# Optimization experiments

Hardware: AMD Instinct MI355X
Metric: run time of the kernel (lower is better)

Reference implementation:

```python
import jax, jax.numpy as jnp
import numpy as np

N, D, V = 16384, 2048, 8192  # rows, code bits, val_range (codebook size)


def setup_inputs() -> dict:
    key = jax.random.key(0)
    k1, k2 = jax.random.split(key)
    x = jax.random.normal(k1, (N, D), dtype=jnp.float32)   # encoded rows
    di = jax.random.normal(k2, (D, V), dtype=jnp.float32)  # decode codebook (fwd.di)
    return {"x": x, "di": di}


def reference(x, di):
    # Original loops over rows doing (1,D)@(D,V) then argmax; batched this is one
    # GEMM [N,D]@[D,V] -> [N,V] followed by argmax over the V axis, cast to float32
    # (the torch code stores the index into a float32 output tensor).
    scores = jnp.matmul(x, di)                  # [N, V]
    return jnp.argmax(scores, axis=1).astype(jnp.float32)  # [N]
```

## Files before the change

### kernel.cpp

```cpp
#include <hip/hip_runtime.h>

typedef _Float16 f16x8 __attribute__((ext_vector_type(8)));
typedef float f32x4 __attribute__((ext_vector_type(4)));
typedef float f32x16 __attribute__((ext_vector_type(16)));
typedef int i32x4 __attribute__((ext_vector_type(4)));
typedef int i32x8 __attribute__((ext_vector_type(8)));

__device__ __forceinline__ unsigned int fkey(float f) {
    unsigned int u = __float_as_uint(f);
    return u ^ ((u & 0x80000000u) ? 0xFFFFFFFFu : 0x80000000u);
}
__device__ __forceinline__ float unkey(unsigned int k) {
    unsigned int u = (k & 0x80000000u) ? (k ^ 0x80000000u) : ~k;
    return __uint_as_float(u);
}

__device__ __forceinline__ unsigned int f32_to_e4m3(float f) {
    float a = fabsf(f);
    a = fminf(a, 448.0f);
    unsigned int s = (__float_as_uint(f) >> 24) & 0x80u;
    if (a < 0.015625f) {
        int m = (int)rintf(a * 512.0f);
        return s | (unsigned int)m;
    }
    int e = ilogbf(a);
    float step = ldexpf(1.0f, e - 3);
    int q = (int)rintf(a / step);
    if (q == 16) { e += 1; q = 8; }
    return s | (unsigned int)(((e + 7) << 3) | (q - 8));
}

__global__ __launch_bounds__(256) void prep_x_q(
    const float* __restrict__ x, unsigned char* __restrict__ Xq)
{
    size_t base = ((size_t)blockIdx.x * 256 + threadIdx.x) * 8;
    float4 a0 = *(const float4*)(x + base);
    float4 a1 = *(const float4*)(x + base + 4);
    float v[8] = {a0.x, a0.y, a0.z, a0.w, a1.x, a1.y, a1.z, a1.w};
    unsigned long long b = 0;
#pragma unroll
    for (int j = 0; j < 8; ++j)
        b |= (unsigned long long)f32_to_e4m3(v[j]) << (8 * j);
    *(unsigned long long*)(Xq + base) = b;
}

__global__ __launch_bounds__(256) void prep_di_q(
    const float* __restrict__ di, unsigned char* __restrict__ DqT,
    _Float16* __restrict__ DhT, _Float16* __restrict__ DlT, int D, int V)
{
    int v  = blockIdx.x * 64 + (threadIdx.x & 63);
    int d0 = blockIdx.y * 32 + (threadIdx.x >> 6) * 8;
    f16x8 h, l;
    unsigned long long b = 0;
#pragma unroll
    for (int j = 0; j < 8; ++j) {
        float val = di[(size_t)(d0 + j) * V + v];
        _Float16 hh = (_Float16)val;
        h[j] = hh;
        l[j] = (_Float16)(val - (float)hh);
        b |= (unsigned long long)f32_to_e4m3(val) << (8 * j);
    }
    *(unsigned long long*)(DqT + (size_t)v * D + d0) = b;
    *(f16x8*)(DhT + (size_t)v * D + d0) = h;
    *(f16x8*)(DlT + (size_t)v * D + d0) = l;
}

__global__ __launch_bounds__(512, 1) void gemm_mx_top2(
    const unsigned char* __restrict__ Xq, const unsigned char* __restrict__ DqT,
    unsigned long long* __restrict__ cand, int N, int D, int V)
{
    __shared__ __align__(16) unsigned char sm[65536];

    const int tid = threadIdx.x;
    const int w = tid >> 6, lane = tid & 63;
    const int wr = w >> 2, wc = w & 3;
    const int l31 = lane & 31, hl = lane >> 5;

    const int cpx = gridDim.x >> 3;
    const int swz = (blockIdx.x & 7) * cpx + (blockIdx.x >> 3);
    const int bm = (swz >> 5) * 256;
    const int bn = (swz & 31) * 256;

    const int srow_in = lane >> 2;
    const int sp      = lane & 3;
    auto stage = [&](int buf, int k0) {
#pragma unroll
        for (int i = 0; i < 4; ++i) {
            const int g = w * 4 + i;
            const int op = g >> 4;
            const int c  = g & 15;
            const int row = c * 16 + srow_in;
            const int slog = sp ^ ((row >> 1) & 3);
            const unsigned char* src =
                (op ? DqT + (size_t)(bn + row) * D : Xq + (size_t)(bm + row) * D)
                + k0 + slog * 16;
            __builtin_amdgcn_global_load_lds(
                (const __attribute__((address_space(1))) void*)src,
                (__attribute__((address_space(3))) void*)
                    (sm + buf * 32768 + op * 16384 + c * 1024),
                16, 0, 0);
        }
    };
    auto ldfrag = [&](int buf, int op, int r) -> i32x8 {
        const unsigned char* base =
            sm + buf * 32768 + op * 16384 + (r >> 4) * 1024 + (r & 15) * 64;
        const int sw = (r >> 1) & 3;
        i32x4 lo = *(const i32x4*)(base + (((hl << 1)    ) ^ sw) * 16);
        i32x4 hi = *(const i32x4*)(base + (((hl << 1) | 1) ^ sw) * 16);
        return __builtin_shufflevector(lo, hi, 0, 1, 2, 3, 4, 5, 6, 7);
    };

    f32x16 acc[4][2];
#pragma unroll
    for (int fm = 0; fm < 4; ++fm)
#pragma unroll
        for (int fn = 0; fn < 2; ++fn)
#pragma unroll
            for (int q = 0; q < 16; ++q) acc[fm][fn][q] = 0.0f;

    const int nt = D / 64;
    int cb = 0;

    stage(0, 0);
    __syncthreads();

#pragma unroll 1
    for (int t = 0; t < nt; ++t) {
        if (t + 1 < nt) stage(cb ^ 1, (t + 1) * 64);

        i32x8 b0 = ldfrag(cb, 1, wc * 64 + 0 * 32 + l31);
        i32x8 b1 = ldfrag(cb, 1, wc * 64 + 1 * 32 + l31);
#pragma unroll
        for (int fm = 0; fm < 4; ++fm) {
            i32x8 a = ldfrag(cb, 0, wr * 128 + fm * 32 + l31);
            acc[fm][0] = __builtin_amdgcn_mfma_scale_f32_32x32x64_f8f6f4(
                a, b0, acc[fm][0], 0, 0, 0, 0x7F7F7F7F, 0, 0x7F7F7F7F);
            acc[fm][1] = __builtin_amdgcn_mfma_scale_f32_32x32x64_f8f6f4(
                a, b1, acc[fm][1], 0, 0, 0, 0x7F7F7F7F, 0, 0x7F7F7F7F);
        }
        __syncthreads();
        cb ^= 1;
    }

    const int nblk = V >> 8;
    const int blkn = bn >> 8;
#pragma unroll
    for (int fm = 0; fm < 4; ++fm)
#pragma unroll
        for (int j = 0; j < 16; ++j) {
            const int row = bm + wr * 128 + fm * 32 + (j & 3) + 8 * (j >> 2) + 4 * hl;
            const int c0 = bn + wc * 64 + l31;
            unsigned long long p0 =
                ((unsigned long long)fkey(acc[fm][0][j]) << 32) |
                (unsigned long long)(0xFFFFFFFFu - (unsigned int)c0);
            unsigned long long p1 =
                ((unsigned long long)fkey(acc[fm][1][j]) << 32) |
                (unsigned long long)(0xFFFFFFFFu - (unsigned int)(c0 + 32));
            unsigned long long t1 = p0 > p1 ? p0 : p1;
            unsigned long long t2 = p0 > p1 ? p1 : p0;
#pragma unroll
            for (int m = 1; m < 32; m <<= 1) {
                unsigned long long o1 = __shfl_xor(t1, m);
                unsigned long long o2 = __shfl_xor(t2, m);
                unsigned long long n1 = t1 > o1 ? t1 : o1;
                unsigned long long lo = t1 > o1 ? o1 : t1;
                unsigned long long m2 = t2 > o2 ? t2 : o2;
                t2 = lo > m2 ? lo : m2;
                t1 = n1;
            }
            if (l31 == 0) {
                size_t ci = (((size_t)row * nblk + blkn) * 4 + wc) * 2;
                cand[ci] = t1;
                cand[ci + 1] = t2;
            }
        }
}

#define DELTA 16.5f

__global__ __launch_bounds__(256) void refine_kernel(
    const unsigned long long* __restrict__ cand,
    const float* __restrict__ X,
    const _Float16* __restrict__ DhT, const _Float16* __restrict__ DlT,
    float* __restrict__ out, int N, int D, int V)
{
    const int w = threadIdx.x >> 6, lane = threadIdx.x & 63;
    const int r = blockIdx.x * 4 + w;
    if (r >= N) return;

    const int nent = (V >> 8) * 8;
    const unsigned long long* cr = cand + (size_t)r * nent;

    unsigned long long p[4];
#pragma unroll
    for (int i = 0; i < 4; ++i) p[i] = cr[lane * 4 + i];

    unsigned long long pmax = p[0];
#pragma unroll
    for (int i = 1; i < 4; ++i) if (p[i] > pmax) pmax = p[i];
#pragma unroll
    for (int m = 1; m < 64; m <<= 1) {
        unsigned long long o = __shfl_xor(pmax, m);
        if (o > pmax) pmax = o;
    }

    const float s1 = unkey((unsigned int)(pmax >> 32));
    const unsigned int kthr = fkey(s1 - DELTA);

    int cnt = 0;
    unsigned long long masks[4];
#pragma unroll
    for (int i = 0; i < 4; ++i) {
        masks[i] = __ballot((unsigned int)(p[i] >> 32) >= kthr);
        cnt += __popcll(masks[i]);
    }

    if (cnt <= 1) {
        if (lane == 0)
            out[r] = (float)(0xFFFFFFFFu - (unsigned int)(pmax & 0xFFFFFFFFull));
        return;
    }

    const float* xrow = X + (size_t)r * D;
    float xbuf[32];
#pragma unroll
    for (int q = 0; q < 8; ++q) {
        float4 xv = *(const float4*)(xrow + lane * 32 + q * 4);
        xbuf[q * 4 + 0] = xv.x; xbuf[q * 4 + 1] = xv.y;
        xbuf[q * 4 + 2] = xv.z; xbuf[q * 4 + 3] = xv.w;
    }

    unsigned long long bestp = 0;
    for (int i = 0; i < 4; ++i) {
        unsigned long long mask = masks[i];
        while (mask) {
            const int src = __ffsll((unsigned long long)mask) - 1;
            mask &= mask - 1;
            const unsigned long long cp = __shfl(p[i], src);
            const int col = (int)(0xFFFFFFFFu - (unsigned int)(cp & 0xFFFFFFFFull));

            const f16x8* dh = (const f16x8*)(DhT + (size_t)col * D) + lane * 4;
            const f16x8* dl = (const f16x8*)(DlT + (size_t)col * D) + lane * 4;
            float s = 0.0f;
#pragma unroll
            for (int q = 0; q < 4; ++q) {
                f16x8 h = dh[q], l = dl[q];
#pragma unroll
                for (int e = 0; e < 8; ++e)
                    s = fmaf(xbuf[q * 8 + e], (float)h[e] + (float)l[e], s);
            }
#pragma unroll
            for (int m = 1; m < 64; m <<= 1) s += __shfl_xor(s, m);

            const unsigned long long pp =
                ((unsigned long long)fkey(s) << 32) |
                (unsigned long long)(0xFFFFFFFFu - (unsigned int)col);
            if (pp > bestp) bestp = pp;
        }
    }
    if (lane == 0)
        out[r] = (float)(0xFFFFFFFFu - (unsigned int)(bestp & 0xFFFFFFFFull));
}

#define FBK 16
#define FTM 8
#define FTN 8

__global__ __launch_bounds__(256) void gemm_argmax_fp32_kernel(
    const float* __restrict__ A, const float* __restrict__ B,
    unsigned long long* __restrict__ best, int N, int D, int V)
{
    __shared__ float As[FBK][128 + 4];
    __shared__ float Bs[FBK][128 + 4];

    const int tid = threadIdx.x;
    const int tx = tid & 15;
    const int ty = tid >> 4;
    const int bm = blockIdx.y * 128;
    const int bn = blockIdx.x * 128;

    const int arow  = tid >> 2;
    const int acol4 = tid & 3;
    const int brow  = tid >> 5;
    const int bcol4 = tid & 31;

    float acc[FTM][FTN];
#pragma unroll
    for (int i = 0; i < FTM; ++i)
#pragma unroll
        for (int j = 0; j < FTN; ++j) acc[i][j] = 0.0f;

    for (int k0 = 0; k0 < D; k0 += FBK) {
        float4 a0 = *reinterpret_cast<const float4*>(&A[(size_t)(bm + arow) * D + k0 + acol4 * 4]);
        float4 a1 = *reinterpret_cast<const float4*>(&A[(size_t)(bm + arow + 64) * D + k0 + acol4 * 4]);
        float4 b0 = *reinterpret_cast<const float4*>(&B[(size_t)(k0 + brow) * V + bn + bcol4 * 4]);
        float4 b1 = *reinterpret_cast<const float4*>(&B[(size_t)(k0 + brow + 8) * V + bn + bcol4 * 4]);

        As[acol4 * 4 + 0][arow] = a0.x;
        As[acol4 * 4 + 1][arow] = a0.y;
        As[acol4 * 4 + 2][arow] = a0.z;
        As[acol4 * 4 + 3][arow] = a0.w;
        As[acol4 * 4 + 0][arow + 64] = a1.x;
        As[acol4 * 4 + 1][arow + 64] = a1.y;
        As[acol4 * 4 + 2][arow + 64] = a1.z;
        As[acol4 * 4 + 3][arow + 64] = a1.w;
        *reinterpret_cast<float4*>(&Bs[brow][bcol4 * 4]) = b0;
        *reinterpret_cast<float4*>(&Bs[brow + 8][bcol4 * 4]) = b1;

        __syncthreads();
#pragma unroll
        for (int kk = 0; kk < FBK; ++kk) {
            float4 av0 = *reinterpret_cast<const float4*>(&As[kk][ty * FTM]);
            float4 av1 = *reinterpret_cast<const float4*>(&As[kk][ty * FTM + 4]);
            float4 bv0 = *reinterpret_cast<const float4*>(&Bs[kk][tx * FTN]);
            float4 bv1 = *reinterpret_cast<const float4*>(&Bs[kk][tx * FTN + 4]);
            float a[FTM] = {av0.x, av0.y, av0.z, av0.w, av1.x, av1.y, av1.z, av1.w};
            float b[FTN] = {bv0.x, bv0.y, bv0.z, bv0.w, bv1.x, bv1.y, bv1.z, bv1.w};
#pragma unroll
            for (int i = 0; i < FTM; ++i)
#pragma unroll
                for (int j = 0; j < FTN; ++j)
                    acc[i][j] = fmaf(a[i], b[j], acc[i][j]);
        }
        __syncthreads();
    }

#pragma unroll
    for (int i = 0; i < FTM; ++i) {
        float bv = acc[i][0];
        int bc = bn + tx * FTN;
#pragma unroll
        for (int j = 1; j < FTN; ++j) {
            float v = acc[i][j];
            int c = bn + tx * FTN + j;
            if (v > bv) { bv = v; bc = c; }
        }
        unsigned long long packed =
            ((unsigned long long)fkey(bv) << 32) |
            (unsigned long long)(0xFFFFFFFFu - (unsigned int)bc);
#pragma unroll
        for (int m = 1; m < 16; m <<= 1) {
            unsigned long long o = __shfl_xor(packed, m, 16);
            if (o > packed) packed = o;
        }
        if (tx == 0) atomicMax(&best[bm + ty * FTM + i], packed);
    }
}

__global__ void decode_kernel(const unsigned long long* __restrict__ best,
                              float* __restrict__ out, int N)
{
    int i = blockIdx.x * blockDim.x + threadIdx.x;
    if (i < N) {
        unsigned int inv = (unsigned int)(best[i] & 0xFFFFFFFFull);
        out[i] = (float)(0xFFFFFFFFu - inv);
    }
}

extern "C" void kernel_launch(void* const* d_in, const int* in_sizes, int n_in,
                              void* d_out, int out_size, void* d_ws, size_t ws_size,
                              hipStream_t stream) {
    const float* A = (const float*)d_in[0];
    const float* B = (const float*)d_in[1];
    float* out = (float*)d_out;

    const int N = out_size;
    const int D = in_sizes[0] / N;
    const int V = in_sizes[1] / D;

    const size_t szXq = (size_t)N * D;
    const size_t szDq = (size_t)D * V;
    const size_t szDh = (size_t)D * V * sizeof(_Float16);
    const size_t candsz = (size_t)N * (V / 256) * 4 * 2 * 8;
    const size_t need = szXq + szDq + 2 * szDh + candsz;

    if (ws_size >= need) {
        char* wsp = (char*)d_ws;
        unsigned char* Xq  = (unsigned char*)(wsp);
        unsigned char* DqT = (unsigned char*)(wsp + szXq);
        _Float16* DhT = (_Float16*)(wsp + szXq + szDq);
        _Float16* DlT = (_Float16*)(wsp + szXq + szDq + szDh);
        unsigned long long* cand =
            (unsigned long long*)(wsp + szXq + szDq + 2 * szDh);

        prep_x_q<<<(int)(((size_t)N * D) / (256 * 8)), 256, 0, stream>>>(A, Xq);
        prep_di_q<<<dim3(V / 64, D / 32), 256, 0, stream>>>(B, DqT, DhT, DlT, D, V);
        gemm_mx_top2<<<(N / 256) * (V / 256), 512, 0, stream>>>(
            Xq, DqT, cand, N, D, V);
        refine_kernel<<<(N + 3) / 4, 256, 0, stream>>>(
            cand, A, DhT, DlT, out, N, D, V);
    } else {
        unsigned long long* best = (unsigned long long*)d_ws;
        hipMemsetAsync(best, 0, (size_t)N * sizeof(unsigned long long), stream);
        gemm_argmax_fp32_kernel<<<dim3(V / 128, N / 128), 256, 0, stream>>>(A, B, best, N, D, V);
        decode_kernel<<<(N + 255) / 256, 256, 0, stream>>>(best, out, N);
    }
}
```

Before: 737.4 us.

## Triple-buffer FP8 GEMM LDS stages with interleaved MFMA phases and barriers

Moves the MX-FP8 GEMM from a double-buffered to a triple-buffered LDS pipeline (96KB dynamic shared memory), prefetching two K-tiles ahead and splitting each tile's loads into halves spread across the MFMA groups. The inner loop is broken into four phases, each pairing an LDS fragment load with two MFMAs, separated by barriers, explicit waitcnts, sched_barriers and s_setprio, so that global-to-LDS traffic overlaps compute and waves interleave. Source addresses are precomputed once. The change also hardcodes the candidate count per row (256) in refine and the workspace size, which only holds for V=8192, and it adds many barriers per iteration that could stall waves.

```diff
diff --git a/kernel.cpp b/kernel.cpp
--- a/kernel.cpp
+++ b/kernel.cpp
@@ -69,7 +69,7 @@
     const unsigned char* __restrict__ Xq, const unsigned char* __restrict__ DqT,
     unsigned long long* __restrict__ cand, int N, int D, int V)
 {
-    __shared__ __align__(16) unsigned char sm[65536];
+    extern __shared__ __align__(16) unsigned char sm[];
 
     const int tid = threadIdx.x;
     const int w = tid >> 6, lane = tid & 63;
@@ -83,21 +83,28 @@
 
     const int srow_in = lane >> 2;
     const int sp      = lane & 3;
-    auto stage = [&](int buf, int k0) {
-#pragma unroll
-        for (int i = 0; i < 4; ++i) {
-            const int g = w * 4 + i;
-            const int op = g >> 4;
-            const int c  = g & 15;
-            const int row = c * 16 + srow_in;
-            const int slog = sp ^ ((row >> 1) & 3);
-            const unsigned char* src =
-                (op ? DqT + (size_t)(bn + row) * D : Xq + (size_t)(bm + row) * D)
-                + k0 + slog * 16;
+
+    const unsigned char* srcbase[4];
+    int dstoff[4];
+#pragma unroll
+    for (int i = 0; i < 4; ++i) {
+        const int g = w * 4 + i;
+        const int op = g >> 4;
+        const int c  = g & 15;
+        const int row = c * 16 + srow_in;
+        const int slog = sp ^ ((row >> 1) & 3);
+        srcbase[i] = (op ? DqT + (size_t)(bn + row) * D
+                         : Xq + (size_t)(bm + row) * D) + slog * 16;
+        dstoff[i] = op * 16384 + c * 1024;
+    }
+
+    auto stageH = [&](int buf, int k0, int h) {
+#pragma unroll
+        for (int i = 2 * h; i < 2 * h + 2; ++i) {
             __builtin_amdgcn_global_load_lds(
-                (const __attribute__((address_space(1))) void*)src,
+                (const __attribute__((address_space(1))) void*)(srcbase[i] + k0),
                 (__attribute__((address_space(3))) void*)
-                    (sm + buf * 32768 + op * 16384 + c * 1024),
+                    (sm + buf * 32768 + dstoff[i]),
                 16, 0, 0);
         }
     };
@@ -119,27 +126,77 @@
             for (int q = 0; q < 16; ++q) acc[fm][fn][q] = 0.0f;
 
     const int nt = D / 64;
-    int cb = 0;
-
-    stage(0, 0);
-    __syncthreads();
+    int cur = 0;
+
+    stageH(0, 0, 0);  stageH(0, 0, 1);
+    stageH(1, 64, 0); stageH(1, 64, 1);
+    asm volatile("s_waitcnt vmcnt(4)" ::: "memory");
+    __builtin_amdgcn_s_barrier();
 
 #pragma unroll 1
     for (int t = 0; t < nt; ++t) {
-        if (t + 1 < nt) stage(cb ^ 1, (t + 1) * 64);
-
-        i32x8 b0 = ldfrag(cb, 1, wc * 64 + 0 * 32 + l31);
-        i32x8 b1 = ldfrag(cb, 1, wc * 64 + 1 * 32 + l31);
-#pragma unroll
-        for (int fm = 0; fm < 4; ++fm) {
-            i32x8 a = ldfrag(cb, 0, wr * 128 + fm * 32 + l31);
-            acc[fm][0] = __builtin_amdgcn_mfma_scale_f32_32x32x64_f8f6f4(
-                a, b0, acc[fm][0], 0, 0, 0, 0x7F7F7F7F, 0, 0x7F7F7F7F);
-            acc[fm][1] = __builtin_amdgcn_mfma_scale_f32_32x32x64_f8f6f4(
-                a, b1, acc[fm][1], 0, 0, 0, 0x7F7F7F7F, 0, 0x7F7F7F7F);
-        }
-        __syncthreads();
-        cb ^= 1;
+        const int fut = (cur >= 1) ? cur - 1 : 2;
+
+        i32x8 b0 = ldfrag(cur, 1, wc * 64 + l31);
+        i32x8 b1 = ldfrag(cur, 1, wc * 64 + 32 + l31);
+        i32x8 a0 = ldfrag(cur, 0, wr * 128 + l31);
+        if (t + 2 < nt) stageH(fut, (t + 2) * 64, 0);
+        __builtin_amdgcn_s_barrier();
+        asm volatile("s_waitcnt lgkmcnt(0)" ::: "memory");
+        __builtin_amdgcn_sched_barrier(0);
+        __builtin_amdgcn_s_setprio(1);
+        acc[0][0] = __builtin_amdgcn_mfma_scale_f32_32x32x64_f8f6f4(
+            a0, b0, acc[0][0], 0, 0, 0, 0x7F7F7F7F, 0, 0x7F7F7F7F);
+        acc[0][1] = __builtin_amdgcn_mfma_scale_f32_32x32x64_f8f6f4(
+            a0, b1, acc[0][1], 0, 0, 0, 0x7F7F7F7F, 0, 0x7F7F7F7F);
+        __builtin_amdgcn_s_setprio(0);
+        __builtin_amdgcn_s_barrier();
+
+        i32x8 a1 = ldfrag(cur, 0, wr * 128 + 32 + l31);
+        __builtin_amdgcn_s_barrier();
+        asm volatile("s_waitcnt lgkmcnt(0)" ::: "memory");
+        __builtin_amdgcn_sched_barrier(0);
+        __builtin_amdgcn_s_setprio(1);
+        acc[1][0] = __builtin_amdgcn_mfma_scale_f32_32x32x64_f8f6f4(
+            a1, b0, acc[1][0], 0, 0, 0, 0x7F7F7F7F, 0, 0x7F7F7F7F);
+        acc[1][1] = __builtin_amdgcn_mfma_scale_f32_32x32x64_f8f6f4(
+            a1, b1, acc[1][1], 0, 0, 0, 0x7F7F7F7F, 0, 0x7F7F7F7F);
+        __builtin_amdgcn_s_setprio(0);
+        __builtin_amdgcn_s_barrier();
+
+        i32x8 a2 = ldfrag(cur, 0, wr * 128 + 64 + l31);
+        if (t + 2 < nt) stageH(fut, (t + 2) * 64, 1);
+        __builtin_amdgcn_s_barrier();
+        asm volatile("s_waitcnt lgkmcnt(0)" ::: "memory");
+        __builtin_amdgcn_sched_barrier(0);
+        __builtin_amdgcn_s_setprio(1);
+        acc[2][0] = __builtin_amdgcn_mfma_scale_f32_32x32x64_f8f6f4(
+            a2, b0, acc[2][0], 0, 0, 0, 0x7F7F7F7F, 0, 0x7F7F7F7F);
+        acc[2][1] = __builtin_amdgcn_mfma_scale_f32_32x32x64_f8f6f4(
+            a2, b1, acc[2][1], 0, 0, 0, 0x7F7F7F7F, 0, 0x7F7F7F7F);
+        __builtin_amdgcn_s_setprio(0);
+        __builtin_amdgcn_s_barrier();
+
+        i32x8 a3 = ldfrag(cur, 0, wr * 128 + 96 + l31);
+        __builtin_amdgcn_s_barrier();
+        asm volatile("s_waitcnt lgkmcnt(0)" ::: "memory");
+        __builtin_amdgcn_sched_barrier(0);
+        __builtin_amdgcn_s_setprio(1);
+        acc[3][0] = __builtin_amdgcn_mfma_scale_f32_32x32x64_f8f6f4(
+            a3, b0, acc[3][0], 0, 0, 0, 0x7F7F7F7F, 0, 0x7F7F7F7F);
+        acc[3][1] = __builtin_amdgcn_mfma_scale_f32_32x32x64_f8f6f4(
+            a3, b1, acc[3][1], 0, 0, 0, 0x7F7F7F7F, 0, 0x7F7F7F7F);
+        __builtin_amdgcn_s_setprio(0);
+        if (t + 1 < nt) {
+            if (t + 2 < nt) {
+                asm volatile("s_waitcnt vmcnt(4)" ::: "memory");
+            } else {
+                asm volatile("s_waitcnt vmcnt(0)" ::: "memory");
+            }
+            __builtin_amdgcn_s_barrier();
+        }
+
+        cur = (cur == 2) ? 0 : cur + 1;
     }
 
     const int nblk = V >> 8;
@@ -188,7 +245,7 @@
     const int r = blockIdx.x * 4 + w;
     if (r >= N) return;
 
-    const int nent = (V >> 8) * 8;
+    const int nent = 256;
     const unsigned long long* cr = cand + (size_t)r * nent;
 
     unsigned long long p[4];
@@ -371,7 +428,7 @@
     const size_t szXq = (size_t)N * D;
     const size_t szDq = (size_t)D * V;
     const size_t szDh = (size_t)D * V * sizeof(_Float16);
-    const size_t candsz = (size_t)N * (V / 256) * 4 * 2 * 8;
+    const size_t candsz = (size_t)N * 256 * 8;
     const size_t need = szXq + szDq + 2 * szDh + candsz;
 
     if (ws_size >= need) {
@@ -383,9 +440,16 @@
         unsigned long long* cand =
             (unsigned long long*)(wsp + szXq + szDq + 2 * szDh);
 
+        static int attr_done = 0;
+        if (!attr_done) {
+            hipFuncSetAttribute((const void*)gemm_mx_top2,
+                                hipFuncAttributeMaxDynamicSharedMemorySize, 98304);
+            attr_done = 1;
+        }
+
         prep_x_q<<<(int)(((size_t)N * D) / (256 * 8)), 256, 0, stream>>>(A, Xq);
         prep_di_q<<<dim3(V / 64, D / 32), 256, 0, stream>>>(B, DqT, DhT, DlT, D, V);
-        gemm_mx_top2<<<(N / 256) * (V / 256), 512, 0, stream>>>(
+        gemm_mx_top2<<<(N / 256) * (V / 256), 512, 98304, stream>>>(
             Xq, DqT, cand, N, D, V);
         refine_kernel<<<(N + 3) / 4, 256, 0, stream>>>(
             cand, A, DhT, DlT, out, N, D, V);
```

New measurement: 750.1 us. About the same (+1.7%).
